# Kernel optimization log

Measured on AMD Instinct MI355X. Metric: run time of the kernel, lower is better.

Reference implementation:

```python
import jax, jax.numpy as jnp
import numpy as np

N_NODES = 15000
N_EDGES = 30000
NUM_GRAPHS = 600
N_STEMS = 6000
N_JBONDS = 3000
DIM = 64
NUM_FEAT = 14
NUM_OUT_PER_STEM = 105


def _lin(a, w, b):
    return a @ w.T + b


def _forward(x, edge_attr, lin0_w, lin0_b, en1_w, en1_b, en2_w, en2_b, root_w, conv_b,
             gru_w_ih, gru_w_hh, gru_b_ih, gru_b_hh, s1_w, s1_b, s2_w, s2_b,
             j1_w, j1_b, j2_w, j2_b, lstm_w_ih, lstm_w_hh, lstm_b_ih, lstm_b_hh,
             lout_w, lout_b, edge_index, stem_atmidx, jbond_atmidx, batch):
    n, dim = x.shape[0], lin0_w.shape[0]
    lrelu = jax.nn.leaky_relu  # negative_slope=0.01 as in torch default
    src, dst = edge_index[0], edge_index[1]

    out = lrelu(_lin(x, lin0_w, lin0_b))
    h = out  # GRU hidden state [N, dim]

    # Edge-conditioned weights (NNConv): small MLP on edge_attr -> [E, dim, dim]
    We = _lin(lrelu(_lin(edge_attr, en1_w, en1_b)), en2_w, en2_b).reshape(-1, dim, dim)
    deg = jnp.clip(jax.ops.segment_sum(jnp.ones_like(dst, dtype=x.dtype), dst, num_segments=n), 1.0)

    for _ in range(6):
        # gather source features, per-edge matvec, scatter-mean to destinations
        msg = jnp.einsum('ei,eio->eo', out[src], We)
        agg = jax.ops.segment_sum(msg, dst, num_segments=n) / deg[:, None]
        m = lrelu(agg + out @ root_w + conv_b)
        # GRUCell (torch gate order: r, z, n)
        gi = _lin(m, gru_w_ih, gru_b_ih)
        gh = _lin(h, gru_w_hh, gru_b_hh)
        ir, iz, inn = jnp.split(gi, 3, axis=-1)
        hr, hz, hn = jnp.split(gh, 3, axis=-1)
        r = jax.nn.sigmoid(ir + hr)
        z = jax.nn.sigmoid(iz + hz)
        ng = jnp.tanh(inn + r * hn)
        h = (1.0 - z) * ng + z * h
        out = h

    stem_preds = _lin(lrelu(_lin(out[stem_atmidx], s1_w, s1_b)), s2_w, s2_b)
    jb = _lin(lrelu(_lin(out[jbond_atmidx.reshape(-1)], j1_w, j1_b)), j2_w, j2_b)
    jbond_preds = jb.reshape(jbond_atmidx.shape).mean(axis=1)

    # Set2Set with 1 processing step (LSTM input 2*dim -> hidden dim)
    b = NUM_GRAPHS
    q_star = jnp.zeros((b, 2 * dim), x.dtype)
    hl = jnp.zeros((b, dim), x.dtype)
    cl = jnp.zeros((b, dim), x.dtype)
    gates = _lin(q_star, lstm_w_ih, lstm_b_ih) + _lin(hl, lstm_w_hh, lstm_b_hh)
    i_, f_, g_, o_ = jnp.split(gates, 4, axis=-1)  # torch LSTM gate order i,f,g,o
    c = jax.nn.sigmoid(f_) * cl + jax.nn.sigmoid(i_) * jnp.tanh(g_)
    q = jax.nn.sigmoid(o_) * jnp.tanh(c)
    e = (out * q[batch]).sum(axis=-1)  # [N]
    emax = jax.ops.segment_max(e, batch, num_segments=b)
    a_un = jnp.exp(e - emax[batch])
    a = a_un / jax.ops.segment_sum(a_un, batch, num_segments=b)[batch]
    r_pool = jax.ops.segment_sum(a[:, None] * out, batch, num_segments=b)
    q_star = jnp.concatenate([q, r_pool], axis=-1)  # [B, 2*dim]

    final = _lin(q_star, lout_w, lout_b)  # [B, 2]
    return final, stem_preds, jbond_preds


def setup_inputs() -> dict:
    key = jax.random.key(0)
    ks = jax.random.split(key, 40)
    d = DIM

    def rn(k, shape, s=0.1):
        return jax.random.normal(k, shape, dtype=jnp.float32) * s

    inp = {}
    inp['x'] = jax.random.normal(ks[0], (N_NODES, NUM_FEAT), dtype=jnp.float32)
    inp['edge_attr'] = jax.random.uniform(ks[1], (N_EDGES, 4), dtype=jnp.float32)
    inp['lin0_w'] = rn(ks[2], (d, NUM_FEAT)); inp['lin0_b'] = rn(ks[3], (d,))
    inp['en1_w'] = rn(ks[4], (d, 4)); inp['en1_b'] = rn(ks[5], (d,))
    inp['en2_w'] = rn(ks[6], (d * d, d), 0.02); inp['en2_b'] = rn(ks[7], (d * d,), 0.02)
    inp['root_w'] = rn(ks[8], (d, d)); inp['conv_b'] = rn(ks[9], (d,))
    inp['gru_w_ih'] = rn(ks[10], (3 * d, d)); inp['gru_w_hh'] = rn(ks[11], (3 * d, d))
    inp['gru_b_ih'] = rn(ks[12], (3 * d,)); inp['gru_b_hh'] = rn(ks[13], (3 * d,))
    inp['s1_w'] = rn(ks[14], (d, d)); inp['s1_b'] = rn(ks[15], (d,))
    inp['s2_w'] = rn(ks[16], (NUM_OUT_PER_STEM, d)); inp['s2_b'] = rn(ks[17], (NUM_OUT_PER_STEM,))
    inp['j1_w'] = rn(ks[18], (d, d)); inp['j1_b'] = rn(ks[19], (d,))
    inp['j2_w'] = rn(ks[20], (1, d)); inp['j2_b'] = rn(ks[21], (1,))
    inp['lstm_w_ih'] = rn(ks[22], (4 * d, 2 * d)); inp['lstm_w_hh'] = rn(ks[23], (4 * d, d))
    inp['lstm_b_ih'] = rn(ks[24], (4 * d,)); inp['lstm_b_hh'] = rn(ks[25], (4 * d,))
    inp['lout_w'] = rn(ks[26], (2, 2 * d)); inp['lout_b'] = rn(ks[27], (2,))
    inp['edge_index'] = jax.random.randint(ks[28], (2, N_EDGES), 0, N_NODES)
    inp['stem_atmidx'] = jax.random.randint(ks[29], (N_STEMS,), 0, N_NODES)
    inp['jbond_atmidx'] = jax.random.randint(ks[30], (N_JBONDS, 2), 0, N_NODES)
    inp['batch'] = jnp.sort(jax.random.randint(ks[31], (N_NODES,), 0, NUM_GRAPHS))
    return inp


def reference(x, edge_attr, lin0_w, lin0_b, en1_w, en1_b, en2_w, en2_b, root_w, conv_b,
              gru_w_ih, gru_w_hh, gru_b_ih, gru_b_hh, s1_w, s1_b, s2_w, s2_b,
              j1_w, j1_b, j2_w, j2_b, lstm_w_ih, lstm_w_hh, lstm_b_ih, lstm_b_hh,
              lout_w, lout_b, edge_index, stem_atmidx, jbond_atmidx, batch):
    return _forward(x, edge_attr, lin0_w, lin0_b, en1_w, en1_b, en2_w, en2_b, root_w, conv_b,
                    gru_w_ih, gru_w_hh, gru_b_ih, gru_b_hh, s1_w, s1_b, s2_w, s2_b,
                    j1_w, j1_b, j2_w, j2_b, lstm_w_ih, lstm_w_hh, lstm_b_ih, lstm_b_hh,
                    lout_w, lout_b, edge_index, stem_atmidx, jbond_atmidx, batch)
```

## Files before the change

### kernel.cpp

```cpp
#include <hip/hip_runtime.h>

typedef unsigned short u16;
typedef unsigned int   u32;

#define N_NODES    15000
#define PADN       15008
#define N_EDGES    30000
#define NUM_GRAPHS 600
#define N_STEMS    6000
#define N_JBONDS   3000

#define OUT_FINAL  0
#define OUT_STEM   1200
#define OUT_JB     631200

#define A1S 68
#define N_CVT 26

#define EBLK 32
#define EGRIDE 938
#define KCH 130
#define A1LS 66
#define RS   66

#define NGROUPS (PADN/16)
#define NWTILES 28
#define HS 72

#define PACK_W2B_N (KCH*2048)
#define PACK_NW_N  (NWTILES*4*512)
#define PACK_HD_N  1792
#define PACK_TOTAL (PACK_W2B_N + PACK_NW_N + PACK_HD_N)

typedef short frag8 __attribute__((ext_vector_type(8)));
typedef float facc4 __attribute__((ext_vector_type(4)));

__device__ __forceinline__ float u2f(u16 v){ union{u32 i; float f;} c; c.i=((u32)v)<<16; return c.f; }
__device__ __forceinline__ float blo(u32 x){ union{u32 i; float f;} c; c.i=x<<16; return c.f; }
__device__ __forceinline__ float bhi(u32 x){ union{u32 i; float f;} c; c.i=x&0xffff0000u; return c.f; }
__device__ __forceinline__ u16  f2b(float f){ union{float f; u32 u;} c; c.f=f; u32 u=c.u;
                                              return (u16)((u + 0x7fffu + ((u>>16)&1u))>>16); }
__device__ __forceinline__ float lrelu(float x){ return x>0.f ? x : 0.01f*x; }
__device__ __forceinline__ float sigmoidf(float x){ return 1.f/(1.f+expf(-x)); }

__device__ __forceinline__ int lower_bound_i(const int* __restrict__ a, int n, int v){
  int lo=0, hi=n;
  while(lo<hi){ int m=(lo+hi)>>1; if(a[m]<v) lo=m+1; else hi=m; }
  return lo;
}

__device__ __forceinline__ void store_out(void* dout, int isf, int idx, float v){
  if(isf) ((float*)dout)[idx] = v;
  else    ((u16*)dout)[idx]   = f2b(v);
}

__device__ __forceinline__ frag8 pack4(uint4 v, float av){
  union { u32 d[4]; frag8 f; } au;
  u32 dd0 = v.x, dd1 = v.y, dd2 = v.z, dd3 = v.w;
  {
    float plo = blo(dd0)*av, phi = bhi(dd0)*av;
    au.d[0] = __builtin_amdgcn_perm(__float_as_uint(phi)+0x8000u,
                                    __float_as_uint(plo)+0x8000u, 0x07060302u);
  }
  {
    float plo = blo(dd1)*av, phi = bhi(dd1)*av;
    au.d[1] = __builtin_amdgcn_perm(__float_as_uint(phi)+0x8000u,
                                    __float_as_uint(plo)+0x8000u, 0x07060302u);
  }
  {
    float plo = blo(dd2)*av, phi = bhi(dd2)*av;
    au.d[2] = __builtin_amdgcn_perm(__float_as_uint(phi)+0x8000u,
                                    __float_as_uint(plo)+0x8000u, 0x07060302u);
  }
  {
    float plo = blo(dd3)*av, phi = bhi(dd3)*av;
    au.d[3] = __builtin_amdgcn_perm(__float_as_uint(phi)+0x8000u,
                                    __float_as_uint(plo)+0x8000u, 0x07060302u);
  }
  return au.f;
}

__global__ __launch_bounds__(256) void k_sniff(const u16* __restrict__ x, int n, int* __restrict__ flag,
                                               float* __restrict__ deg, float* __restrict__ agg,
                                               float* __restrict__ outF, u16* __restrict__ outB){
  int tid = blockIdx.x*256 + threadIdx.x;
  int stride = gridDim.x*256;
  int local = 0;
  for(int i = tid; i < n; i += stride){
    u16 v = x[i];
    if(((v>>7)&0xFFu) == 0xFFu) local = 1;
  }
  if(local) atomicOr(flag, 1);
  float4 z = (float4){0.f,0.f,0.f,0.f};
  for(int i = tid; i < PADN; i += stride) deg[i] = 0.f;
  for(int i = tid; i < PADN*64/4; i += stride) ((float4*)agg)[i] = z;
  for(int i = tid; i < (PADN-N_NODES)*64/4; i += stride) ((float4*)(outF + (size_t)N_NODES*64))[i] = z;
  for(int i = tid; i < (PADN-N_NODES)*64/8; i += stride) ((float4*)(outB + (size_t)N_NODES*64))[i] = z;
}

struct CvtArgs { const void* src[N_CVT]; float* dst[N_CVT]; int n[N_CVT]; };

__global__ __launch_bounds__(256) void k_cvt(CvtArgs A, const int* __restrict__ flag){
  int isf = *flag;
  int tid = blockIdx.x*256 + threadIdx.x;
  int stride = gridDim.x*256;
  for(int b=0; b<N_CVT; b++){
    int n = A.n[b];
    const float* sf = (const float*)A.src[b];
    const u16*   sb = (const u16*)A.src[b];
    float* d = A.dst[b];
    for(int i=tid; i<n; i+=stride) d[i] = isf ? sf[i] : u2f(sb[i]);
  }
}

__global__ __launch_bounds__(64) void k_lin0(const float* __restrict__ x, const float* __restrict__ w,
                                             const float* __restrict__ b,
                                             float* __restrict__ outF, u16* __restrict__ outB){
  int n = blockIdx.x, o = threadIdx.x;
  __shared__ float xs[14];
  if(o<14) xs[o] = x[n*14+o];
  __syncthreads();
  float acc = b[o];
  #pragma unroll
  for(int i=0;i<14;i++) acc += xs[i]*w[o*14+i];
  float v = lrelu(acc);
  outF[n*64+o] = v;
  outB[n*64+o] = f2b(v);
}

__global__ __launch_bounds__(128) void k_a1(const float* __restrict__ ea,
                                            const float* __restrict__ en1w, const float* __restrict__ en1b,
                                            u16* __restrict__ a1b,
                                            const int* __restrict__ ei, float* __restrict__ deg){
  int e = blockIdx.x, k = threadIdx.x;
  if(k >= A1S) return;
  float v = 0.f;
  if(k < 64){
    float acc = en1b[k];
    #pragma unroll
    for(int c=0;c<4;c++) acc += ea[e*4+c] * en1w[k*4+c];
    v = lrelu(acc);
  } else if(k == 64) v = 1.0f;
  a1b[e*A1S + k] = f2b(v);
  if(k == 65) atomicAdd(&deg[ei[N_EDGES + e]], 1.0f);
}

__global__ __launch_bounds__(256) void k_packAll(const float* __restrict__ en2w, const float* __restrict__ en2b,
                                                 u16* __restrict__ B2b,
                                                 const float* __restrict__ rootw, const float* __restrict__ wih,
                                                 const float* __restrict__ whh, u16* __restrict__ gBn,
                                                 const float* __restrict__ s1w, const float* __restrict__ s2w,
                                                 const float* __restrict__ j1w,
                                                 float4* __restrict__ s1P, float4* __restrict__ s2P,
                                                 float4* __restrict__ j1P){
  int idx = blockIdx.x*256 + threadIdx.x;
  if(idx < PACK_W2B_N){
    int jj  = idx & 7;
    int l   = (idx >> 3) & 63;
    int nt  = (idx >> 9) & 3;
    int c   = idx >> 11;
    int q = l >> 4, m16 = l & 15;
    int kidx = c*32 + q*8 + jj;
    int k = kidx >> 6, j = kidx & 63;
    int o = nt*16 + m16;
    float v = (k < 64) ? en2w[((size_t)(j*64 + o))*64 + k] : en2b[j*64 + o];
    B2b[idx] = f2b(v);
    return;
  }
  idx -= PACK_W2B_N;
  if(idx < PACK_NW_N){
    int jj = idx & 7, l = (idx>>3) & 63, ch = (idx>>9) & 3, t = idx >> 11;
    int m16 = l & 15, q = l >> 4;
    int j = ((ch & 1) ? 32 : 0) + q*8 + jj;
    float v;
    if(t < 4){        int o = t*16 + m16;        v = rootw[j*64 + o]; }
    else if(t < 16){  int g = (t-4)*16 + m16;    v = wih[(size_t)g*64 + j]; }
    else {            int g = (t-16)*16 + m16;   v = whh[(size_t)g*64 + j]; }
    u16 hb = f2b(v);
    gBn[idx] = (ch >> 1) ? f2b(v - u2f(hb)) : hb;
    return;
  }
  idx -= PACK_NW_N;
  if(idx < PACK_HD_N){
    if(idx < 1024){
      int o = idx & 63, j4 = idx >> 6;
      const float* r = s1w + o*64 + 4*j4;
      s1P[idx] = (float4){r[0], r[1], r[2], r[3]};
      const float* r2 = j1w + o*64 + 4*j4;
      j1P[idx] = (float4){r2[0], r2[1], r2[2], r2[3]};
    }
    {
      int j4 = idx / 112, t = idx % 112;
      float4 v = {0.f,0.f,0.f,0.f};
      if(t < 105){
        const float* r = s2w + t*64 + 4*j4;
        v = (float4){r[0], r[1], r[2], r[3]};
      }
      s2P[idx] = v;
    }
  }
}

__global__ __launch_bounds__(256, 3) void k_egemm(const u16* __restrict__ outB,
                                               const u16* __restrict__ a1b,
                                               const u16* __restrict__ B2b,
                                               const int* __restrict__ ei,
                                               float* __restrict__ agg){
  int tid = threadIdx.x;
  int l = tid & 63, w = tid >> 6;
  int m16 = l & 15, q = l >> 4;
  int eb = blockIdx.x * EBLK;

  __shared__ __align__(16) u16 a1l[EBLK*A1LS];
  __shared__ __align__(16) float red[4][EBLK*RS];

  int e0 = eb + m16, e1 = eb + 16 + m16;
  int n0 = (e0 < N_EDGES) ? ei[e0] : 0;
  int n1 = (e1 < N_EDGES) ? ei[e1] : 0;
  uint4 o200 = *(const uint4*)(outB + (size_t)n0*64 +      q*8);
  uint4 o201 = *(const uint4*)(outB + (size_t)n0*64 + 32 + q*8);
  uint4 o210 = *(const uint4*)(outB + (size_t)n1*64 +      q*8);
  uint4 o211 = *(const uint4*)(outB + (size_t)n1*64 + 32 + q*8);

  for(int idx = tid; idx < EBLK*33; idx += 256){
    int r = idx / 33, c = idx - r*33;
    int e = eb + r;
    u32 v = (e < N_EDGES) ? ((const u32*)(a1b + (size_t)e*A1S))[c] : 0u;
    ((u32*)a1l)[r*33 + c] = v;
  }
  __syncthreads();

  facc4 acc[2][4];
  #pragma unroll
  for(int t=0;t<2;t++)
    #pragma unroll
    for(int nt=0;nt<4;nt++) acc[t][nt] = (facc4){0.f,0.f,0.f,0.f};

  int ks = (w*65) >> 2, ke = ((w+1)*65) >> 2;
  const frag8* __restrict__ Bg = (const frag8*)B2b;

  frag8 bE0[4], bO0[4], bE1[4], bO1[4];
  #pragma unroll
  for(int nt=0;nt<4;nt++){
    bE0[nt] = Bg[(size_t)(2*ks  )*256 + nt*64 + l];
    bO0[nt] = Bg[(size_t)(2*ks+1)*256 + nt*64 + l];
  }

#define COMPUTE(KK, BE, BO)                                                          \
  {                                                                                  \
    float av0 = u2f(a1l[m16*A1LS + (KK)]);                                           \
    float av1 = u2f(a1l[(16+m16)*A1LS + (KK)]);                                      \
    {                                                                                \
      frag8 aE0 = pack4(o200, av0);                                                  \
      frag8 aE1 = pack4(o210, av1);                                                  \
      _Pragma("unroll")                                                              \
      for(int nt=0;nt<4;nt++)                                                        \
        acc[0][nt] = __builtin_amdgcn_mfma_f32_16x16x32_bf16(aE0, BE[nt], acc[0][nt], 0,0,0); \
      _Pragma("unroll")                                                              \
      for(int nt=0;nt<4;nt++)                                                        \
        acc[1][nt] = __builtin_amdgcn_mfma_f32_16x16x32_bf16(aE1, BE[nt], acc[1][nt], 0,0,0); \
    }                                                                                \
    {                                                                                \
      frag8 aO0 = pack4(o201, av0);                                                  \
      frag8 aO1 = pack4(o211, av1);                                                  \
      _Pragma("unroll")                                                              \
      for(int nt=0;nt<4;nt++)                                                        \
        acc[0][nt] = __builtin_amdgcn_mfma_f32_16x16x32_bf16(aO0, BO[nt], acc[0][nt], 0,0,0); \
      _Pragma("unroll")                                                              \
      for(int nt=0;nt<4;nt++)                                                        \
        acc[1][nt] = __builtin_amdgcn_mfma_f32_16x16x32_bf16(aO1, BO[nt], acc[1][nt], 0,0,0); \
    }                                                                                \
  }

  for(int k = ks; k < ke; k += 2){
    int k1 = (k+1 < ke) ? k+1 : k;
    #pragma unroll
    for(int nt=0;nt<4;nt++){
      bE1[nt] = Bg[(size_t)(2*k1  )*256 + nt*64 + l];
      bO1[nt] = Bg[(size_t)(2*k1+1)*256 + nt*64 + l];
    }
    COMPUTE(k, bE0, bO0);
    int k2 = (k+2 < ke) ? k+2 : k;
    #pragma unroll
    for(int nt=0;nt<4;nt++){
      bE0[nt] = Bg[(size_t)(2*k2  )*256 + nt*64 + l];
      bO0[nt] = Bg[(size_t)(2*k2+1)*256 + nt*64 + l];
    }
    if(k+1 < ke) COMPUTE(k+1, bE1, bO1);
  }
#undef COMPUTE

  #pragma unroll
  for(int t = 0; t < 2; t++){
    #pragma unroll
    for(int nt = 0; nt < 4; nt++){
      #pragma unroll
      for(int r = 0; r < 4; r++){
        int el = t*16 + q*4 + r;
        red[w][el*RS + nt*16 + m16] = acc[t][nt][r];
      }
    }
  }
  __syncthreads();

  for(int i = tid; i < EBLK*64; i += 256){
    int el = i >> 6, o = i & 63;
    int e = eb + el;
    if(e < N_EDGES){
      float s = red[0][el*RS + o] + red[1][el*RS + o]
              + red[2][el*RS + o] + red[3][el*RS + o];
      atomicAdd(&agg[(size_t)ei[N_EDGES + e]*64 + o], s);
    }
  }
}

__global__ __launch_bounds__(256) void k_node(float* __restrict__ agg, const float* __restrict__ deg,
                                              float* __restrict__ outF, u16* __restrict__ outB,
                                              const u16* __restrict__ gBn, const float* __restrict__ convb,
                                              const float* __restrict__ bih, const float* __restrict__ bhh){
  int tid = threadIdx.x;
  int l = tid & 63, w = tid >> 6;
  int m16 = l & 15, q = l >> 4;
  int nb = blockIdx.x * 16;

  __shared__ __align__(16) u16 hhi[16][HS], hlo[16][HS];
  __shared__ __align__(16) u16 mhi[16][HS], mlo[16][HS];

  {
    float4 v = ((const float4*)(outF + (size_t)nb*64))[tid];
    int base = tid*4;
    int node = base >> 6, o = base & 63;
    float vv[4] = {v.x, v.y, v.z, v.w};
    #pragma unroll
    for(int t=0;t<4;t++){
      u16 hb = f2b(vv[t]);
      hhi[node][o+t] = hb;
      hlo[node][o+t] = f2b(vv[t] - u2f(hb));
    }
  }
  __syncthreads();

  const frag8* __restrict__ Bg = (const frag8*)gBn;

#define GEMM6(ACC, A0, A1, L0, L1, T)                                      \
  {                                                                        \
    const frag8* bp = Bg + (size_t)(T)*256 + l;                            \
    frag8 b0 = bp[0], b1 = bp[64], b2 = bp[128], b3 = bp[192];             \
    ACC = __builtin_amdgcn_mfma_f32_16x16x32_bf16(A0, b0, ACC, 0,0,0);     \
    ACC = __builtin_amdgcn_mfma_f32_16x16x32_bf16(A1, b1, ACC, 0,0,0);     \
    ACC = __builtin_amdgcn_mfma_f32_16x16x32_bf16(L0, b0, ACC, 0,0,0);     \
    ACC = __builtin_amdgcn_mfma_f32_16x16x32_bf16(L1, b1, ACC, 0,0,0);     \
    ACC = __builtin_amdgcn_mfma_f32_16x16x32_bf16(A0, b2, ACC, 0,0,0);     \
    ACC = __builtin_amdgcn_mfma_f32_16x16x32_bf16(A1, b3, ACC, 0,0,0);     \
  }

  frag8 hA0 = *(const frag8*)&hhi[m16][q*8];
  frag8 hA1 = *(const frag8*)&hhi[m16][32 + q*8];
  frag8 hL0 = *(const frag8*)&hlo[m16][q*8];
  frag8 hL1 = *(const frag8*)&hlo[m16][32 + q*8];

  facc4 dR  = (facc4){0.f,0.f,0.f,0.f};
  facc4 ghA = (facc4){0.f,0.f,0.f,0.f};
  facc4 ghB = (facc4){0.f,0.f,0.f,0.f};
  facc4 ghC = (facc4){0.f,0.f,0.f,0.f};
  GEMM6(dR,  hA0, hA1, hL0, hL1, w);
  GEMM6(ghA, hA0, hA1, hL0, hL1, 16 + w);
  GEMM6(ghB, hA0, hA1, hL0, hL1, 20 + w);
  GEMM6(ghC, hA0, hA1, hL0, hL1, 24 + w);

  int o = w*16 + m16;
  float cb = convb[o];
  #pragma unroll
  for(int r=0;r<4;r++){
    int node = q*4 + r;
    int n = nb + node;
    float a = agg[(size_t)n*64 + o] / fmaxf(deg[n], 1.0f) + dR[r] + cb;
    agg[(size_t)n*64 + o] = 0.f;
    float mv = lrelu(a);
    u16 mb = f2b(mv);
    mhi[node][o] = mb;
    mlo[node][o] = f2b(mv - u2f(mb));
  }
  __syncthreads();

  frag8 mA0 = *(const frag8*)&mhi[m16][q*8];
  frag8 mA1 = *(const frag8*)&mhi[m16][32 + q*8];
  frag8 mL0 = *(const frag8*)&mlo[m16][q*8];
  frag8 mL1 = *(const frag8*)&mlo[m16][32 + q*8];

  facc4 giA = (facc4){0.f,0.f,0.f,0.f};
  facc4 giB = (facc4){0.f,0.f,0.f,0.f};
  facc4 giC = (facc4){0.f,0.f,0.f,0.f};
  GEMM6(giA, mA0, mA1, mL0, mL1, 4 + w);
  GEMM6(giB, mA0, mA1, mL0, mL1, 8 + w);
  GEMM6(giC, mA0, mA1, mL0, mL1, 12 + w);
#undef GEMM6

  float bi0 = bih[o], bi1 = bih[64+o], bi2 = bih[128+o];
  float bh0 = bhh[o], bh1 = bhh[64+o], bh2 = bhh[128+o];
  #pragma unroll
  for(int r=0;r<4;r++){
    int node = q*4 + r;
    int n = nb + node;
    float ir = giA[r]+bi0, iz = giB[r]+bi1, inn = giC[r]+bi2;
    float hr = ghA[r]+bh0, hz = ghB[r]+bh1, hn = ghC[r]+bh2;
    float rr  = sigmoidf(ir + hr);
    float z   = sigmoidf(iz + hz);
    float ngv = tanhf(inn + rr*hn);
    float hold = u2f(hhi[node][o]) + u2f(hlo[node][o]);
    float hnew = (1.f - z)*ngv + z*hold;
    if(n < N_NODES){
      outF[(size_t)n*64 + o] = hnew;
      outB[(size_t)n*64 + o] = f2b(hnew);
    }
  }
}

__global__ __launch_bounds__(512) void k_stem(const float* __restrict__ outF, const int* __restrict__ sidx,
                                              const float4* __restrict__ s1P, const float* __restrict__ s1b,
                                              const float4* __restrict__ s2P, const float* __restrict__ s2b,
                                              void* __restrict__ dout, const int* __restrict__ flag){
  int grp = threadIdx.x >> 7, t = threadIdx.x & 127;
  int s = blockIdx.x*4 + grp;
  int isf = *flag;
  __shared__ __align__(16) float xs[4][64], hid[4][64];
  int a = sidx[s];
  if(t < 64) xs[grp][t] = outF[(size_t)a*64 + t];
  __syncthreads();
  if(t < 64){
    float acc = s1b[t];
    const float4* xp = (const float4*)xs[grp];
    #pragma unroll 8
    for(int j4=0;j4<16;j4++){
      float4 w = s1P[j4*64+t];
      float4 x = xp[j4];
      acc += w.x*x.x + w.y*x.y + w.z*x.z + w.w*x.w;
    }
    hid[grp][t] = lrelu(acc);
  }
  __syncthreads();
  if(t < 105){
    float acc = s2b[t];
    const float4* hp = (const float4*)hid[grp];
    #pragma unroll 8
    for(int j4=0;j4<16;j4++){
      float4 w = s2P[j4*112+t];
      float4 h = hp[j4];
      acc += w.x*h.x + w.y*h.y + w.z*h.z + w.w*h.w;
    }
    store_out(dout, isf, OUT_STEM + s*105 + t, acc);
  }
}

__global__ __launch_bounds__(512) void k_jbond(const float* __restrict__ outF, const int* __restrict__ jidx,
                                               const float4* __restrict__ j1P, const float* __restrict__ j1b,
                                               const float* __restrict__ j2w, const float* __restrict__ j2b,
                                               void* __restrict__ dout, const int* __restrict__ flag){
  int grp = threadIdx.x >> 7, t = threadIdx.x & 127;
  int jb = blockIdx.x*4 + grp;
  int isf = *flag;
  __shared__ __align__(16) float xs[4][2][64], hid[4][2][64];
  int at = t >> 6, k = t & 63;
  int a = jidx[jb*2 + at];
  xs[grp][at][k] = outF[(size_t)a*64 + k];
  __syncthreads();
  {
    float acc = j1b[k];
    const float4* xp = (const float4*)xs[grp][at];
    #pragma unroll 8
    for(int j4=0;j4<16;j4++){
      float4 w = j1P[j4*64+k];
      float4 x = xp[j4];
      acc += w.x*x.x + w.y*x.y + w.z*x.z + w.w*x.w;
    }
    hid[grp][at][k] = lrelu(acc);
  }
  __syncthreads();
  if(t < 64){
    float p = (hid[grp][0][t] + hid[grp][1][t]) * j2w[t];
    #pragma unroll
    for(int s=32;s;s>>=1) p += __shfl_xor(p, s, 64);
    if(t==0) store_out(dout, isf, OUT_JB + jb, 0.5f*p + j2b[0]);
  }
}

__global__ __launch_bounds__(64) void k_s2s(const float* __restrict__ outF, const int* __restrict__ batch,
                                            const float* __restrict__ bih, const float* __restrict__ bhh,
                                            const float* __restrict__ loutw, const float* __restrict__ loutb,
                                            void* __restrict__ dout, const int* __restrict__ flag){
  int b = blockIdx.x, t = threadIdx.x;
  int isf = *flag;
  float i_ = bih[t]     + bhh[t];
  float g_ = bih[128+t] + bhh[128+t];
  float o_ = bih[192+t] + bhh[192+t];
  float c  = sigmoidf(i_)*tanhf(g_);
  float q  = sigmoidf(o_)*tanhf(c);

  int lo = lower_bound_i(batch, N_NODES, b);
  int hi = lower_bound_i(batch, N_NODES, b+1);

  float emax = -3.4e38f;
  for(int n=lo;n<hi;n++){
    float p = outF[n*64+t]*q;
    #pragma unroll
    for(int s=32;s;s>>=1) p += __shfl_xor(p, s, 64);
    emax = fmaxf(emax, p);
  }
  float Z = 0.f, racc = 0.f;
  for(int n=lo;n<hi;n++){
    float v = outF[n*64+t];
    float p = v*q;
    #pragma unroll
    for(int s=32;s;s>>=1) p += __shfl_xor(p, s, 64);
    float w = expf(p - emax);
    Z += w; racc += w*v;
  }
  float rp = (hi>lo) ? racc/Z : 0.f;

  #pragma unroll
  for(int j=0;j<2;j++){
    float p = q*loutw[j*128+t] + rp*loutw[j*128+64+t];
    #pragma unroll
    for(int s=32;s;s>>=1) p += __shfl_xor(p, s, 64);
    if(t==0) store_out(dout, isf, OUT_FINAL + b*2 + j, p + loutb[j]);
  }
}

extern "C" void kernel_launch(void* const* d_in, const int* in_sizes, int n_in,
                              void* d_out, int out_size, void* d_ws, size_t ws_size,
                              hipStream_t stream) {
  const int* edge_index  = (const int*)d_in[28];
  const int* stem_atmidx = (const int*)d_in[29];
  const int* jbond_atmidx= (const int*)d_in[30];
  const int* batch       = (const int*)d_in[31];

  char* ws = (char*)d_ws;
  size_t off = 0;
  auto alloc = [&](size_t bytes)->void*{ void* p = ws + off; off = (off + bytes + 255) & ~(size_t)255; return p; };

  int*   flag = (int*)  alloc(4);
  float* outF = (float*)alloc((size_t)PADN*64*4);
  u16*   outB = (u16*)  alloc((size_t)PADN*64*2);
  float* agg  = (float*)alloc((size_t)PADN*64*4);
  u16*   a1b  = (u16*)  alloc((size_t)N_EDGES*A1S*2);
  u16*   B2b  = (u16*)  alloc((size_t)KCH*2048*2 + 2048*2);
  u16*   gBn  = (u16*)  alloc((size_t)NWTILES*4*512*2);
  float* deg  = (float*)alloc((size_t)PADN*4);
  float4* s1P   = (float4*)alloc(1024*16);
  float4* s2P   = (float4*)alloc(1792*16);
  float4* j1P   = (float4*)alloc(1024*16);

  static const int cvt_idx[N_CVT] = {0,1,2,3,4,5,6,7,8,9,10,11,12,13,14,15,16,17,18,19,20,21,24,25,26,27};
  CvtArgs A;
  float* cF[N_CVT];
  for(int i=0;i<N_CVT;i++){
    int src = cvt_idx[i];
    int n = in_sizes[src];
    cF[i] = (float*)alloc((size_t)n*4);
    A.src[i] = d_in[src];
    A.dst[i] = cF[i];
    A.n[i]   = n;
  }
  (void)ws_size; (void)n_in; (void)out_size;
  float* xF=cF[0];   float* eaF=cF[1];  float* l0w=cF[2];  float* l0b=cF[3];
  float* e1w=cF[4];  float* e1b=cF[5];  float* e2w=cF[6];  float* e2b=cF[7];
  float* rootw=cF[8];float* convb=cF[9];
  float* wih=cF[10]; float* whh=cF[11]; float* bih=cF[12]; float* bhh=cF[13];
  float* s1w=cF[14]; float* s1b=cF[15]; float* s2w=cF[16]; float* s2b=cF[17];
  float* j1w=cF[18]; float* j1b=cF[19]; float* j2w=cF[20]; float* j2b=cF[21];
  float* lbih=cF[22];float* lbhh=cF[23];float* loutw=cF[24];float* loutb=cF[25];

  hipMemsetAsync(flag, 0, 4, stream);

  k_sniff <<<128, 256, 0, stream>>>((const u16*)d_in[0], in_sizes[0], flag, deg, agg, outF, outB);
  k_cvt   <<<512, 256, 0, stream>>>(A, flag);

  k_lin0    <<<N_NODES, 64, 0, stream>>>(xF, l0w, l0b, outF, outB);
  k_a1      <<<N_EDGES, 128, 0, stream>>>(eaF, e1w, e1b, a1b, edge_index, deg);
  k_packAll <<<PACK_TOTAL/256, 256, 0, stream>>>(e2w, e2b, B2b, rootw, wih, whh, gBn,
                                                 s1w, s2w, j1w, s1P, s2P, j1P);

  for(int it=0; it<6; it++){
    k_egemm<<<EGRIDE, 256, 0, stream>>>(outB, a1b, B2b, edge_index, agg);
    k_node <<<NGROUPS, 256, 0, stream>>>(agg, deg, outF, outB, gBn, convb, bih, bhh);
  }

  k_stem <<<N_STEMS/4, 512, 0, stream>>>(outF, stem_atmidx, s1P, s1b, s2P, s2b, d_out, flag);
  k_jbond<<<N_JBONDS/4, 512, 0, stream>>>(outF, jbond_atmidx, j1P, j1b, j2w, j2b, d_out, flag);
  k_s2s  <<<NUM_GRAPHS, 64, 0, stream>>>(outF, batch, lbih, lbhh, loutw, loutb, d_out, flag);
}
```

Baseline: 458.6 us.

## Double edge tile per block to reuse B fragments across four row tiles

Result: slower. 665.9 us (+45.2%).

```diff
diff --git a/kernel.cpp b/kernel.cpp
--- a/kernel.cpp
+++ b/kernel.cpp
@@ -17,8 +17,8 @@
 #define A1S 68
 #define N_CVT 26
 
-#define EBLK 32
-#define EGRIDE 938
+#define EBLK 64
+#define EGRIDE 469
 #define KCH 130
 #define A1LS 66
 #define RS   66
@@ -201,7 +201,7 @@
   }
 }
 
-__global__ __launch_bounds__(256, 3) void k_egemm(const u16* __restrict__ outB,
+__global__ __launch_bounds__(256, 2) void k_egemm(const u16* __restrict__ outB,
                                                const u16* __restrict__ a1b,
                                                const u16* __restrict__ B2b,
                                                const int* __restrict__ ei,
@@ -212,15 +212,22 @@
   int eb = blockIdx.x * EBLK;
 
   __shared__ __align__(16) u16 a1l[EBLK*A1LS];
-  __shared__ __align__(16) float red[4][EBLK*RS];
-
-  int e0 = eb + m16, e1 = eb + 16 + m16;
-  int n0 = (e0 < N_EDGES) ? ei[e0] : 0;
-  int n1 = (e1 < N_EDGES) ? ei[e1] : 0;
-  uint4 o200 = *(const uint4*)(outB + (size_t)n0*64 +      q*8);
-  uint4 o201 = *(const uint4*)(outB + (size_t)n0*64 + 32 + q*8);
-  uint4 o210 = *(const uint4*)(outB + (size_t)n1*64 +      q*8);
-  uint4 o211 = *(const uint4*)(outB + (size_t)n1*64 + 32 + q*8);
+  __shared__ __align__(16) float red[2][EBLK*RS];
+
+  for(int i = tid; i < 2112; i += 256) ((float4*)red)[i] = (float4){0.f,0.f,0.f,0.f};
+
+  int nidx[4];
+  #pragma unroll
+  for(int t=0;t<4;t++){
+    int e = eb + t*16 + m16;
+    nidx[t] = (e < N_EDGES) ? ei[e] : 0;
+  }
+  uint4 oE[4], oO[4];
+  #pragma unroll
+  for(int t=0;t<4;t++){
+    oE[t] = *(const uint4*)(outB + (size_t)nidx[t]*64 +      q*8);
+    oO[t] = *(const uint4*)(outB + (size_t)nidx[t]*64 + 32 + q*8);
+  }
 
   for(int idx = tid; idx < EBLK*33; idx += 256){
     int r = idx / 33, c = idx - r*33;
@@ -230,85 +237,65 @@
   }
   __syncthreads();
 
-  facc4 acc[2][4];
-  #pragma unroll
-  for(int t=0;t<2;t++)
+  facc4 acc[4][4];
+  #pragma unroll
+  for(int t=0;t<4;t++)
     #pragma unroll
     for(int nt=0;nt<4;nt++) acc[t][nt] = (facc4){0.f,0.f,0.f,0.f};
 
   int ks = (w*65) >> 2, ke = ((w+1)*65) >> 2;
   const frag8* __restrict__ Bg = (const frag8*)B2b;
 
-  frag8 bE0[4], bO0[4], bE1[4], bO1[4];
-  #pragma unroll
-  for(int nt=0;nt<4;nt++){
-    bE0[nt] = Bg[(size_t)(2*ks  )*256 + nt*64 + l];
-    bO0[nt] = Bg[(size_t)(2*ks+1)*256 + nt*64 + l];
-  }
-
-#define COMPUTE(KK, BE, BO)                                                          \
-  {                                                                                  \
-    float av0 = u2f(a1l[m16*A1LS + (KK)]);                                           \
-    float av1 = u2f(a1l[(16+m16)*A1LS + (KK)]);                                      \
-    {                                                                                \
-      frag8 aE0 = pack4(o200, av0);                                                  \
-      frag8 aE1 = pack4(o210, av1);                                                  \
-      _Pragma("unroll")                                                              \
-      for(int nt=0;nt<4;nt++)                                                        \
-        acc[0][nt] = __builtin_amdgcn_mfma_f32_16x16x32_bf16(aE0, BE[nt], acc[0][nt], 0,0,0); \
-      _Pragma("unroll")                                                              \
-      for(int nt=0;nt<4;nt++)                                                        \
-        acc[1][nt] = __builtin_amdgcn_mfma_f32_16x16x32_bf16(aE1, BE[nt], acc[1][nt], 0,0,0); \
-    }                                                                                \
-    {                                                                                \
-      frag8 aO0 = pack4(o201, av0);                                                  \
-      frag8 aO1 = pack4(o211, av1);                                                  \
-      _Pragma("unroll")                                                              \
-      for(int nt=0;nt<4;nt++)                                                        \
-        acc[0][nt] = __builtin_amdgcn_mfma_f32_16x16x32_bf16(aO0, BO[nt], acc[0][nt], 0,0,0); \
-      _Pragma("unroll")                                                              \
-      for(int nt=0;nt<4;nt++)                                                        \
-        acc[1][nt] = __builtin_amdgcn_mfma_f32_16x16x32_bf16(aO1, BO[nt], acc[1][nt], 0,0,0); \
-    }                                                                                \
-  }
-
-  for(int k = ks; k < ke; k += 2){
-    int k1 = (k+1 < ke) ? k+1 : k;
-    #pragma unroll
-    for(int nt=0;nt<4;nt++){
-      bE1[nt] = Bg[(size_t)(2*k1  )*256 + nt*64 + l];
-      bO1[nt] = Bg[(size_t)(2*k1+1)*256 + nt*64 + l];
-    }
-    COMPUTE(k, bE0, bO0);
-    int k2 = (k+2 < ke) ? k+2 : k;
-    #pragma unroll
-    for(int nt=0;nt<4;nt++){
-      bE0[nt] = Bg[(size_t)(2*k2  )*256 + nt*64 + l];
-      bO0[nt] = Bg[(size_t)(2*k2+1)*256 + nt*64 + l];
-    }
-    if(k+1 < ke) COMPUTE(k+1, bE1, bO1);
-  }
-#undef COMPUTE
-
-  #pragma unroll
-  for(int t = 0; t < 2; t++){
-    #pragma unroll
-    for(int nt = 0; nt < 4; nt++){
+  frag8 bA[4], bB[4];
+  #pragma unroll
+  for(int nt=0;nt<4;nt++) bA[nt] = Bg[(size_t)(2*ks)*256 + nt*64 + l];
+
+  for(int k = ks; k < ke; ++k){
+    #pragma unroll
+    for(int nt=0;nt<4;nt++) bB[nt] = Bg[(size_t)(2*k+1)*256 + nt*64 + l];
+
+    float av[4];
+    #pragma unroll
+    for(int t=0;t<4;t++) av[t] = u2f(a1l[(t*16 + m16)*A1LS + k]);
+
+    #pragma unroll
+    for(int t=0;t<4;t++){
+      frag8 a = pack4(oE[t], av[t]);
       #pragma unroll
-      for(int r = 0; r < 4; r++){
+      for(int nt=0;nt<4;nt++)
+        acc[t][nt] = __builtin_amdgcn_mfma_f32_16x16x32_bf16(a, bA[nt], acc[t][nt], 0,0,0);
+    }
+
+    int kn = (k+1 < ke) ? (k+1) : k;
+    #pragma unroll
+    for(int nt=0;nt<4;nt++) bA[nt] = Bg[(size_t)(2*kn)*256 + nt*64 + l];
+
+    #pragma unroll
+    for(int t=0;t<4;t++){
+      frag8 a = pack4(oO[t], av[t]);
+      #pragma unroll
+      for(int nt=0;nt<4;nt++)
+        acc[t][nt] = __builtin_amdgcn_mfma_f32_16x16x32_bf16(a, bB[nt], acc[t][nt], 0,0,0);
+    }
+  }
+
+  float* slab = red[w & 1];
+  #pragma unroll
+  for(int t=0;t<4;t++)
+    #pragma unroll
+    for(int nt=0;nt<4;nt++)
+      #pragma unroll
+      for(int r=0;r<4;r++){
         int el = t*16 + q*4 + r;
-        red[w][el*RS + nt*16 + m16] = acc[t][nt][r];
+        atomicAdd(&slab[el*RS + nt*16 + m16], acc[t][nt][r]);
       }
-    }
-  }
   __syncthreads();
 
   for(int i = tid; i < EBLK*64; i += 256){
     int el = i >> 6, o = i & 63;
     int e = eb + el;
     if(e < N_EDGES){
-      float s = red[0][el*RS + o] + red[1][el*RS + o]
-              + red[2][el*RS + o] + red[3][el*RS + o];
+      float s = red[0][el*RS + o] + red[1][el*RS + o];
       atomicAdd(&agg[(size_t)ei[N_EDGES + e]*64 + o], s);
     }
   }
```
